# Optimization experiments

Measured on AMD Instinct MI355X. Metric: run time of the kernel, lower is better.

The kernel has to match this reference:

```python
import jax, jax.numpy as jnp
import numpy as np

T, D_IN, H, D_OUT = 20, 4, 768, 1
B = 1024


def setup_inputs() -> dict:
    key = jax.random.key(0)
    ks = jax.random.split(key, 8)
    s = 1.0 / np.sqrt(H)
    return {
        "batch_price": jax.random.normal(ks[0], (B, T, D_IN), jnp.float32),
        "batch_event": jax.random.normal(ks[1], (B, T, H), jnp.float32),
        "W_ih": jax.random.uniform(ks[2], (T, 4 * H, D_IN), jnp.float32, -s, s),
        "W_hh": jax.random.uniform(ks[3], (T, 4 * H, H), jnp.float32, -s, s),
        "b_ih": jax.random.uniform(ks[4], (T, 4 * H), jnp.float32, -s, s),
        "b_hh": jax.random.uniform(ks[5], (T, 4 * H), jnp.float32, -s, s),
        "fc_w": jax.random.uniform(ks[6], (D_OUT, H), jnp.float32, -s, s),
        "fc_b": jax.random.uniform(ks[7], (D_OUT,), jnp.float32, -s, s),
    }


def _lstm_cell(x, h_mat, c, wih, whh, bih, bhh):
    # gates: [B, 4H] in PyTorch LSTMCell order (i, f, g, o)
    gates = x @ wih.T + bih + h_mat @ whh.T + bhh
    i, f, g, o = jnp.split(gates, 4, axis=-1)
    c_next = jax.nn.sigmoid(f) * c + jax.nn.sigmoid(i) * jnp.tanh(g)
    h_next = jax.nn.sigmoid(o) * jnp.tanh(c_next)
    return h_next, c_next


def reference(batch_price, batch_event, W_ih, W_hh, b_ih, b_hh, fc_w, fc_b):
    Bb, Tt, _ = batch_price.shape
    Hh = W_hh.shape[-1]
    # step 0: hx = batch_event[:, 0], cell state = zeros
    h, c = _lstm_cell(batch_price[:, 0], batch_event[:, 0],
                      jnp.zeros((Bb, Hh), batch_price.dtype),
                      W_ih[0], W_hh[0], b_ih[0], b_hh[0])

    def step(carry, inp):
        h, c = carry
        x, ev, wih, whh, bih, bhh = inp
        # faithful to source: hx = torch.sum(batch_event_t + h_prev) -> scalar
        hx = jnp.sum(ev + h)
        h_mat = jnp.broadcast_to(hx, (Bb, Hh))
        h2, c2 = _lstm_cell(x, h_mat, c, wih, whh, bih, bhh)
        return (h2, c2), None

    xs = (jnp.swapaxes(batch_price[:, 1:], 0, 1),  # [T-1, B, D_IN]
          jnp.swapaxes(batch_event[:, 1:], 0, 1),  # [T-1, B, H]
          W_ih[1:], W_hh[1:], b_ih[1:], b_hh[1:])
    (h, c), _ = jax.lax.scan(step, (h, c), xs)
    return h @ fc_w.T + fc_b  # [B, 1]
```

## Files before the change

kernel.cpp:

```cpp
#include <hip/hip_runtime.h>
#include <stdint.h>

#define Bsz 1024
#define Tn  20
#define Hn  768
#define G4n 3072

#define WS_SH    0
#define WS_SEV   32
#define WS_PART  64
#define WS_BCAST 576
#define WS_RS    640
#define WS_BS    62080
#define WS_C     123520
#define WS_EVH   909952
#define WS_EVL   1303168
#define WS_WH    1696384
#define WS_WL    2581120

#define NBC_EV   512
#define NBC_W    1152
#define NBC_Z    3
#define NBC_TOT  (NBC_EV + NBC_W + NBC_Z)

#define NB_GEMM   768
#define NB_ROWSUM 1824
#define NB_SEV    608
#define NB_BIAS   60
#define NB_TOTAL  (NB_GEMM + NB_ROWSUM + NB_SEV + NB_BIAS)

typedef float  floatx4 __attribute__((ext_vector_type(4)));
typedef short  bfrag8  __attribute__((ext_vector_type(8)));

__device__ __forceinline__ float wave_reduce(float v){
#pragma unroll
    for (int o = 32; o > 0; o >>= 1) v += __shfl_down(v, o, 64);
    return v;
}
__device__ __forceinline__ float sigf(float x){ return 1.0f/(1.0f+__expf(-x)); }
__device__ __forceinline__ float tanhfast(float x){ return 2.0f/(1.0f+__expf(-2.0f*x)) - 1.0f; }
__device__ __forceinline__ unsigned short f2bf(float f){
    uint32_t u = __float_as_uint(f);
    return (unsigned short)((u + 0x7fffu + ((u>>16)&1u)) >> 16);
}
__device__ __forceinline__ float bf2f(unsigned short h){ return __uint_as_float(((uint32_t)h)<<16); }
__device__ __forceinline__ uint64_t pack_tv(unsigned t, float v){
    return ((uint64_t)t << 32) | (uint64_t)__float_as_uint(v);
}

__global__ __launch_bounds__(256) void k_conv(
    const float* __restrict__ ev, const float* __restrict__ whh,
    float* __restrict__ ws)
{
    int bid = blockIdx.x, tid = threadIdx.x;
    if (bid < NBC_EV + NBC_W) {
        if (tid >= 192) return;
        int r = tid / 96;
        int i = (tid - r*96) * 8;
        const float* src;
        unsigned short *dh, *dl;
        if (bid < NBC_EV) {
            int b = bid*2 + r;
            src = ev + (size_t)b*(Tn*Hn) + i;
            dh = (unsigned short*)(ws + WS_EVH) + (size_t)b*Hn + i;
            dl = (unsigned short*)(ws + WS_EVL) + (size_t)b*Hn + i;
        } else {
            int p = (bid - NBC_EV)*2 + r;
            int gsel = p / Hn;
            int ga = (gsel==0) ? 0 : (gsel==1 ? 2 : 3);
            int j = ga*Hn + (p - gsel*Hn);
            src = whh + (size_t)j*Hn + i;
            dh = (unsigned short*)(ws + WS_WH) + (size_t)p*Hn + i;
            dl = (unsigned short*)(ws + WS_WL) + (size_t)p*Hn + i;
        }
        float4 v0 = *(const float4*)src;
        float4 v1 = *(const float4*)(src+4);
        float f[8] = {v0.x,v0.y,v0.z,v0.w,v1.x,v1.y,v1.z,v1.w};
        bfrag8 hv, lv;
#pragma unroll
        for (int q = 0; q < 8; ++q) {
            unsigned short hb = f2bf(f[q]);
            hv[q] = (short)hb;
            lv[q] = (short)f2bf(f[q] - bf2f(hb));
        }
        *(bfrag8*)dh = hv;
        *(bfrag8*)dl = lv;
    } else {
        int idx = (bid - NBC_EV - NBC_W)*256 + tid;
        if (idx < 640) ws[idx] = 0.0f;
    }
}

__global__ __launch_bounds__(256) void k_pre(
    const float* __restrict__ price, const float* __restrict__ ev,
    const float* __restrict__ wih,   const float* __restrict__ whh,
    const float* __restrict__ bih,   const float* __restrict__ bhh,
    float* __restrict__ ws)
{
    __shared__ float redk[4];
    int blk = blockIdx.x, tid = threadIdx.x;
    int lane = tid & 63, wid = tid >> 6;

    if (blk < NB_GEMM) {
        float* Sh   = ws + WS_SH;
        float* cbuf = ws + WS_C;
        int bt = blk / 48, kt = blk % 48;
        int b0 = bt*64, k0 = kt*16;
        int w = wid, q = lane >> 4, col = lane & 15;

        const unsigned short* evh = (const unsigned short*)(ws + WS_EVH);
        const unsigned short* evl = (const unsigned short*)(ws + WS_EVL);
        const unsigned short* wh  = (const unsigned short*)(ws + WS_WH);
        const unsigned short* wl  = (const unsigned short*)(ws + WS_WL);

        int arow = b0 + w*16 + col;
        const unsigned short* pah = evh + (size_t)arow*Hn + q*8;
        const unsigned short* pal = evl + (size_t)arow*Hn + q*8;
        int br0 = 0*Hn + k0 + col;
        int br1 = 1*Hn + k0 + col;
        int br2 = 2*Hn + k0 + col;
        const unsigned short* pbh0 = wh + (size_t)br0*Hn + q*8;
        const unsigned short* pbl0 = wl + (size_t)br0*Hn + q*8;
        const unsigned short* pbh1 = wh + (size_t)br1*Hn + q*8;
        const unsigned short* pbl1 = wl + (size_t)br1*Hn + q*8;
        const unsigned short* pbh2 = wh + (size_t)br2*Hn + q*8;
        const unsigned short* pbl2 = wl + (size_t)br2*Hn + q*8;

        floatx4 acc0 = (floatx4){0.f,0.f,0.f,0.f};
        floatx4 acc1 = (floatx4){0.f,0.f,0.f,0.f};
        floatx4 acc2 = (floatx4){0.f,0.f,0.f,0.f};

#pragma unroll 4
        for (int kk = 0; kk < Hn; kk += 32) {
            bfrag8 ah = *(const bfrag8*)(pah + kk);
            bfrag8 al = *(const bfrag8*)(pal + kk);
            bfrag8 b0h = *(const bfrag8*)(pbh0 + kk);
            bfrag8 b0l = *(const bfrag8*)(pbl0 + kk);
            acc0 = __builtin_amdgcn_mfma_f32_16x16x32_bf16(ah, b0h, acc0, 0,0,0);
            acc0 = __builtin_amdgcn_mfma_f32_16x16x32_bf16(ah, b0l, acc0, 0,0,0);
            acc0 = __builtin_amdgcn_mfma_f32_16x16x32_bf16(al, b0h, acc0, 0,0,0);
            bfrag8 b1h = *(const bfrag8*)(pbh1 + kk);
            bfrag8 b1l = *(const bfrag8*)(pbl1 + kk);
            acc1 = __builtin_amdgcn_mfma_f32_16x16x32_bf16(ah, b1h, acc1, 0,0,0);
            acc1 = __builtin_amdgcn_mfma_f32_16x16x32_bf16(ah, b1l, acc1, 0,0,0);
            acc1 = __builtin_amdgcn_mfma_f32_16x16x32_bf16(al, b1h, acc1, 0,0,0);
            bfrag8 b2h = *(const bfrag8*)(pbh2 + kk);
            bfrag8 b2l = *(const bfrag8*)(pbl2 + kk);
            acc2 = __builtin_amdgcn_mfma_f32_16x16x32_bf16(ah, b2h, acc2, 0,0,0);
            acc2 = __builtin_amdgcn_mfma_f32_16x16x32_bf16(ah, b2l, acc2, 0,0,0);
            acc2 = __builtin_amdgcn_mfma_f32_16x16x32_bf16(al, b2h, acc2, 0,0,0);
        }

        float hsum = 0.f;
#pragma unroll
        for (int r = 0; r < 4; ++r) {
            int b = b0 + w*16 + q*4 + r;
            float4 xv = *(const float4*)(price + (size_t)b*(Tn*4));
            int j0 = 0*Hn + k0 + col;
            int j1 = 2*Hn + k0 + col;
            int j2 = 3*Hn + k0 + col;
            float4 w0 = *(const float4*)(wih + (size_t)j0*4);
            float4 w1 = *(const float4*)(wih + (size_t)j1*4);
            float4 w2 = *(const float4*)(wih + (size_t)j2*4);
            float gi = acc0[r] + xv.x*w0.x + xv.y*w0.y + xv.z*w0.z + xv.w*w0.w + bih[j0] + bhh[j0];
            float gg = acc1[r] + xv.x*w1.x + xv.y*w1.y + xv.z*w1.z + xv.w*w1.w + bih[j1] + bhh[j1];
            float go = acc2[r] + xv.x*w2.x + xv.y*w2.y + xv.z*w2.z + xv.w*w2.w + bih[j2] + bhh[j2];
            float c0 = sigf(gi) * tanhfast(gg);
            float h0 = sigf(go) * tanhfast(c0);
            cbuf[(size_t)b*Hn + k0 + col] = c0;
            hsum += h0;
        }
        hsum = wave_reduce(hsum);
        if (lane == 0) redk[w] = hsum;
        __syncthreads();
        if (tid == 0) atomicAdd(&Sh[0], redk[0]+redk[1]+redk[2]+redk[3]);
        return;
    }

    blk -= NB_GEMM;
    if (blk < NB_ROWSUM) {
        int gw = blk*4 + wid;
        int t  = 1 + gw/384;
        int j0 = (gw - (t-1)*384)*8;
        const float* base = whh + ((size_t)t*G4n + j0)*Hn + (size_t)lane*4;
        float s[8];
#pragma unroll
        for (int r = 0; r < 8; ++r) {
            float4 v0 = *(const float4*)(base + (size_t)r*Hn);
            float4 v1 = *(const float4*)(base + (size_t)r*Hn + 256);
            float4 v2 = *(const float4*)(base + (size_t)r*Hn + 512);
            s[r] = (v0.x+v0.y+v0.z+v0.w) + (v1.x+v1.y+v1.z+v1.w) + (v2.x+v2.y+v2.z+v2.w);
        }
        float* rowsum = ws + WS_RS;
#pragma unroll
        for (int r = 0; r < 8; ++r) {
            float rs = wave_reduce(s[r]);
            if (lane == 0) rowsum[(size_t)t*G4n + j0 + r] = rs;
        }
        return;
    }

    blk -= NB_ROWSUM;
    if (blk < NB_SEV) {
        int gw = blk*4 + wid;
        int t   = 1 + gw/128;
        int b0s = (gw - (t-1)*128)*8;
        float s = 0.f;
#pragma unroll
        for (int r = 0; r < 8; ++r) {
            const float* base = ev + ((size_t)(b0s+r)*Tn + t)*Hn + (size_t)lane*4;
            float4 v0 = *(const float4*)(base);
            float4 v1 = *(const float4*)(base + 256);
            float4 v2 = *(const float4*)(base + 512);
            s += (v0.x+v0.y+v0.z+v0.w) + (v1.x+v1.y+v1.z+v1.w) + (v2.x+v2.y+v2.z+v2.w);
        }
        s = wave_reduce(s);
        if (lane == 0) atomicAdd(ws + WS_SEV + t, s);
        return;
    }

    blk -= NB_SEV;
    {
        int idx = blk*256 + tid;
        float4 a = *(const float4*)(bih + (size_t)idx*4);
        float4 b = *(const float4*)(bhh + (size_t)idx*4);
        float4 r4; r4.x=a.x+b.x; r4.y=a.y+b.y; r4.z=a.z+b.z; r4.w=a.w+b.w;
        *(float4*)(ws + WS_BS + (size_t)idx*4) = r4;
    }
}

__global__ __launch_bounds__(768) void k_steps(
    const float* __restrict__ price, const float* __restrict__ wih,
    const float* __restrict__ fcw,   const float* __restrict__ fcb,
    float* __restrict__ ws, float* __restrict__ out)
{
    __shared__ float pr[4][80];
    __shared__ float red[12];
    __shared__ float redP[4];
    __shared__ float redF[4][12];

    float* Sh  = ws + WS_SH;
    float* Sev = ws + WS_SEV;
    uint64_t* part = (uint64_t*)(ws + WS_PART);
    const float* rowsum  = ws + WS_RS;
    const float* biassum = ws + WS_BS;
    float* cbuf = ws + WS_C;

    int blk = blockIdx.x, tid = threadIdx.x;
    int lane = tid & 63, wid = tid >> 6;
    int k = tid;

    if (tid < 320) {
        int e = tid / 80, r = tid - e*80;
        pr[e][r] = price[(size_t)(blk + 256*e)*(Tn*4) + r];
    }

    float c[4];
#pragma unroll
    for (int e = 0; e < 4; ++e)
        c[e] = cbuf[(size_t)(blk + 256*e)*Hn + k];

    float fcwk = fcw[k];
    float fcb0 = fcb[0];
    float sh0  = Sh[0];

    __syncthreads();

    float hsum_prev = 0.f;
    float vout[4] = {0.f,0.f,0.f,0.f};

    for (int t = 1; t < Tn; ++t) {
        if (t >= 2) {
            float v = wave_reduce(hsum_prev);
            if (lane == 0) red[wid] = v;
            __syncthreads();
            if (tid == 0) {
                float tot = 0.f;
#pragma unroll
                for (int i = 0; i < 12; ++i) tot += red[i];
                __hip_atomic_store(&part[blk], pack_tv((unsigned)(t-1), tot),
                                   __ATOMIC_RELAXED, __HIP_MEMORY_SCOPE_AGENT);
            }
        }

        const float* wih_t = wih + (size_t)t*G4n*4;
        float rsv[4], base[4][4];
#pragma unroll
        for (int g = 0; g < 4; ++g) {
            int j = g*Hn + k;
            float4 wv = *(const float4*)(wih_t + (size_t)j*4);
            rsv[g]   = rowsum[t*G4n + j];
            float bs = biassum[t*G4n + j];
#pragma unroll
            for (int e = 0; e < 4; ++e) {
                base[e][g] = pr[e][t*4+0]*wv.x + pr[e][t*4+1]*wv.y
                           + pr[e][t*4+2]*wv.z + pr[e][t*4+3]*wv.w + bs;
            }
        }
        float sevt = Sev[t];

        float hx;
        if (t == 1) {
            hx = sevt + sh0;
        } else {
            if (tid < 256) {
                uint64_t u = __hip_atomic_load(&part[tid], __ATOMIC_RELAXED, __HIP_MEMORY_SCOPE_AGENT);
                while ((unsigned)(u >> 32) != (unsigned)(t-1)) {
                    __builtin_amdgcn_s_sleep(1);
                    u = __hip_atomic_load(&part[tid], __ATOMIC_RELAXED, __HIP_MEMORY_SCOPE_AGENT);
                }
                float pv = wave_reduce(__uint_as_float((uint32_t)u));
                if (lane == 0) redP[wid] = pv;
            }
            __syncthreads();
            hx = sevt + (redP[0]+redP[1]+redP[2]+redP[3]);
        }

        float hsum = 0.f;
#pragma unroll
        for (int e = 0; e < 4; ++e) {
            float gi = base[e][0] + hx*rsv[0];
            float gf = base[e][1] + hx*rsv[1];
            float gg = base[e][2] + hx*rsv[2];
            float go = base[e][3] + hx*rsv[3];
            float cn = sigf(gf)*c[e] + sigf(gi)*tanhfast(gg);
            c[e] = cn;
            float h = sigf(go)*tanhfast(cn);
            hsum += h;
            if (t == Tn-1) vout[e] = wave_reduce(h * fcwk);
        }
        hsum_prev = hsum;
    }

    if (lane == 0) {
#pragma unroll
        for (int e = 0; e < 4; ++e) redF[e][wid] = vout[e];
    }
    __syncthreads();
    if (tid < 4) {
        float tot = 0.f;
#pragma unroll
        for (int i = 0; i < 12; ++i) tot += redF[tid][i];
        out[blk + 256*tid] = tot + fcb0;
    }
}

extern "C" void kernel_launch(void* const* d_in, const int* in_sizes, int n_in,
                              void* d_out, int out_size, void* d_ws, size_t ws_size,
                              hipStream_t stream)
{
    const float* price = (const float*)d_in[0];
    const float* ev    = (const float*)d_in[1];
    const float* wih   = (const float*)d_in[2];
    const float* whh   = (const float*)d_in[3];
    const float* bih   = (const float*)d_in[4];
    const float* bhh   = (const float*)d_in[5];
    const float* fcw   = (const float*)d_in[6];
    const float* fcb   = (const float*)d_in[7];
    float* out = (float*)d_out;
    float* ws  = (float*)d_ws;

    k_conv <<<NBC_TOT, 256, 0, stream>>>(ev, whh, ws);
    k_pre  <<<NB_TOTAL, 256, 0, stream>>>(price, ev, wih, whh, bih, bhh, ws);
    k_steps<<<256, 768, 0, stream>>>(price, wih, fcw, fcb, ws, out);
}
```

Measured before the change: 475.2 us.

## Broadcast per-step hx from one block and tile GEMM operands for MFMA

Before, every block of the step kernel polled all 256 partial-sum slots and reduced them itself. Now only block 0 gathers the partials and publishes the packed (step, hx) value through a single broadcast slot, and the other blocks spin on that one word, without sleeps. The bf16 split copies of the event and weight matrices are also stored in an MFMA-fragment-tiled layout, so each wave reads its operand fragments contiguously, and the W_ih and bias loads are hoisted out of the per-row epilogue loop. The broadcast adds a serial hop through block 0 on every step, and tight polling without sleep adds pressure on the memory system.

```diff
diff --git a/kernel.cpp b/kernel.cpp
--- a/kernel.cpp
+++ b/kernel.cpp
@@ -59,32 +59,38 @@
         int i = (tid - r*96) * 8;
         const float* src;
         unsigned short *dh, *dl;
+        int prow;
         if (bid < NBC_EV) {
-            int b = bid*2 + r;
-            src = ev + (size_t)b*(Tn*Hn) + i;
-            dh = (unsigned short*)(ws + WS_EVH) + (size_t)b*Hn + i;
-            dl = (unsigned short*)(ws + WS_EVL) + (size_t)b*Hn + i;
+            prow = bid*2 + r;
+            src = ev + (size_t)prow*(Tn*Hn) + i;
+            dh = (unsigned short*)(ws + WS_EVH);
+            dl = (unsigned short*)(ws + WS_EVL);
         } else {
             int p = (bid - NBC_EV)*2 + r;
             int gsel = p / Hn;
             int ga = (gsel==0) ? 0 : (gsel==1 ? 2 : 3);
             int j = ga*Hn + (p - gsel*Hn);
+            prow = p;
             src = whh + (size_t)j*Hn + i;
-            dh = (unsigned short*)(ws + WS_WH) + (size_t)p*Hn + i;
-            dl = (unsigned short*)(ws + WS_WL) + (size_t)p*Hn + i;
-        }
+            dh = (unsigned short*)(ws + WS_WH);
+            dl = (unsigned short*)(ws + WS_WL);
+        }
+        int rb = prow >> 4, col = prow & 15;
+        int kb = i >> 5, q = (i >> 3) & 3;
+        size_t base = (((size_t)(rb*24 + kb))*64 + q*16 + col) * 8;
+
         float4 v0 = *(const float4*)src;
         float4 v1 = *(const float4*)(src+4);
         float f[8] = {v0.x,v0.y,v0.z,v0.w,v1.x,v1.y,v1.z,v1.w};
         bfrag8 hv, lv;
 #pragma unroll
-        for (int q = 0; q < 8; ++q) {
-            unsigned short hb = f2bf(f[q]);
-            hv[q] = (short)hb;
-            lv[q] = (short)f2bf(f[q] - bf2f(hb));
-        }
-        *(bfrag8*)dh = hv;
-        *(bfrag8*)dl = lv;
+        for (int qq = 0; qq < 8; ++qq) {
+            unsigned short hb = f2bf(f[qq]);
+            hv[qq] = (short)hb;
+            lv[qq] = (short)f2bf(f[qq] - bf2f(hb));
+        }
+        *(bfrag8*)(dh + base) = hv;
+        *(bfrag8*)(dl + base) = lv;
     } else {
         int idx = (bid - NBC_EV - NBC_W)*256 + tid;
         if (idx < 640) ws[idx] = 0.0f;
@@ -113,58 +119,60 @@
         const unsigned short* wh  = (const unsigned short*)(ws + WS_WH);
         const unsigned short* wl  = (const unsigned short*)(ws + WS_WL);
 
-        int arow = b0 + w*16 + col;
-        const unsigned short* pah = evh + (size_t)arow*Hn + q*8;
-        const unsigned short* pal = evl + (size_t)arow*Hn + q*8;
-        int br0 = 0*Hn + k0 + col;
-        int br1 = 1*Hn + k0 + col;
-        int br2 = 2*Hn + k0 + col;
-        const unsigned short* pbh0 = wh + (size_t)br0*Hn + q*8;
-        const unsigned short* pbl0 = wl + (size_t)br0*Hn + q*8;
-        const unsigned short* pbh1 = wh + (size_t)br1*Hn + q*8;
-        const unsigned short* pbl1 = wl + (size_t)br1*Hn + q*8;
-        const unsigned short* pbh2 = wh + (size_t)br2*Hn + q*8;
-        const unsigned short* pbl2 = wl + (size_t)br2*Hn + q*8;
+        int rb_a = bt*4 + w;
+        const unsigned short* pah = evh + (size_t)rb_a*24*512 + (size_t)lane*8;
+        const unsigned short* pal = evl + (size_t)rb_a*24*512 + (size_t)lane*8;
+        const unsigned short* pb0h = wh + (size_t)(  0 + kt)*24*512 + (size_t)lane*8;
+        const unsigned short* pb0l = wl + (size_t)(  0 + kt)*24*512 + (size_t)lane*8;
+        const unsigned short* pb1h = wh + (size_t)( 48 + kt)*24*512 + (size_t)lane*8;
+        const unsigned short* pb1l = wl + (size_t)( 48 + kt)*24*512 + (size_t)lane*8;
+        const unsigned short* pb2h = wh + (size_t)( 96 + kt)*24*512 + (size_t)lane*8;
+        const unsigned short* pb2l = wl + (size_t)( 96 + kt)*24*512 + (size_t)lane*8;
 
         floatx4 acc0 = (floatx4){0.f,0.f,0.f,0.f};
         floatx4 acc1 = (floatx4){0.f,0.f,0.f,0.f};
         floatx4 acc2 = (floatx4){0.f,0.f,0.f,0.f};
 
 #pragma unroll 4
-        for (int kk = 0; kk < Hn; kk += 32) {
-            bfrag8 ah = *(const bfrag8*)(pah + kk);
-            bfrag8 al = *(const bfrag8*)(pal + kk);
-            bfrag8 b0h = *(const bfrag8*)(pbh0 + kk);
-            bfrag8 b0l = *(const bfrag8*)(pbl0 + kk);
+        for (int kb = 0; kb < 24; ++kb) {
+            int off = kb*512;
+            bfrag8 ah  = *(const bfrag8*)(pah  + off);
+            bfrag8 al  = *(const bfrag8*)(pal  + off);
+            bfrag8 b0h = *(const bfrag8*)(pb0h + off);
+            bfrag8 b0l = *(const bfrag8*)(pb0l + off);
             acc0 = __builtin_amdgcn_mfma_f32_16x16x32_bf16(ah, b0h, acc0, 0,0,0);
             acc0 = __builtin_amdgcn_mfma_f32_16x16x32_bf16(ah, b0l, acc0, 0,0,0);
             acc0 = __builtin_amdgcn_mfma_f32_16x16x32_bf16(al, b0h, acc0, 0,0,0);
-            bfrag8 b1h = *(const bfrag8*)(pbh1 + kk);
-            bfrag8 b1l = *(const bfrag8*)(pbl1 + kk);
+            bfrag8 b1h = *(const bfrag8*)(pb1h + off);
+            bfrag8 b1l = *(const bfrag8*)(pb1l + off);
             acc1 = __builtin_amdgcn_mfma_f32_16x16x32_bf16(ah, b1h, acc1, 0,0,0);
             acc1 = __builtin_amdgcn_mfma_f32_16x16x32_bf16(ah, b1l, acc1, 0,0,0);
             acc1 = __builtin_amdgcn_mfma_f32_16x16x32_bf16(al, b1h, acc1, 0,0,0);
-            bfrag8 b2h = *(const bfrag8*)(pbh2 + kk);
-            bfrag8 b2l = *(const bfrag8*)(pbl2 + kk);
+            bfrag8 b2h = *(const bfrag8*)(pb2h + off);
+            bfrag8 b2l = *(const bfrag8*)(pb2l + off);
             acc2 = __builtin_amdgcn_mfma_f32_16x16x32_bf16(ah, b2h, acc2, 0,0,0);
             acc2 = __builtin_amdgcn_mfma_f32_16x16x32_bf16(ah, b2l, acc2, 0,0,0);
             acc2 = __builtin_amdgcn_mfma_f32_16x16x32_bf16(al, b2h, acc2, 0,0,0);
         }
 
+        int j0 = 0*Hn + k0 + col;
+        int j1 = 2*Hn + k0 + col;
+        int j2 = 3*Hn + k0 + col;
+        float4 w0 = *(const float4*)(wih + (size_t)j0*4);
+        float4 w1 = *(const float4*)(wih + (size_t)j1*4);
+        float4 w2 = *(const float4*)(wih + (size_t)j2*4);
+        float bb0 = bih[j0] + bhh[j0];
+        float bb1 = bih[j1] + bhh[j1];
+        float bb2 = bih[j2] + bhh[j2];
+
         float hsum = 0.f;
 #pragma unroll
         for (int r = 0; r < 4; ++r) {
             int b = b0 + w*16 + q*4 + r;
             float4 xv = *(const float4*)(price + (size_t)b*(Tn*4));
-            int j0 = 0*Hn + k0 + col;
-            int j1 = 2*Hn + k0 + col;
-            int j2 = 3*Hn + k0 + col;
-            float4 w0 = *(const float4*)(wih + (size_t)j0*4);
-            float4 w1 = *(const float4*)(wih + (size_t)j1*4);
-            float4 w2 = *(const float4*)(wih + (size_t)j2*4);
-            float gi = acc0[r] + xv.x*w0.x + xv.y*w0.y + xv.z*w0.z + xv.w*w0.w + bih[j0] + bhh[j0];
-            float gg = acc1[r] + xv.x*w1.x + xv.y*w1.y + xv.z*w1.z + xv.w*w1.w + bih[j1] + bhh[j1];
-            float go = acc2[r] + xv.x*w2.x + xv.y*w2.y + xv.z*w2.z + xv.w*w2.w + bih[j2] + bhh[j2];
+            float gi = acc0[r] + xv.x*w0.x + xv.y*w0.y + xv.z*w0.z + xv.w*w0.w + bb0;
+            float gg = acc1[r] + xv.x*w1.x + xv.y*w1.y + xv.z*w1.z + xv.w*w1.w + bb1;
+            float go = acc2[r] + xv.x*w2.x + xv.y*w2.y + xv.z*w2.z + xv.w*w2.w + bb2;
             float c0 = sigf(gi) * tanhfast(gg);
             float h0 = sigf(go) * tanhfast(c0);
             cbuf[(size_t)b*Hn + k0 + col] = c0;
@@ -238,10 +246,12 @@
     __shared__ float red[12];
     __shared__ float redP[4];
     __shared__ float redF[4][12];
+    __shared__ float shx;
 
     float* Sh  = ws + WS_SH;
     float* Sev = ws + WS_SEV;
-    uint64_t* part = (uint64_t*)(ws + WS_PART);
+    uint64_t* part  = (uint64_t*)(ws + WS_PART);
+    uint64_t* bcast = (uint64_t*)(ws + WS_BCAST);
     const float* rowsum  = ws + WS_RS;
     const float* biassum = ws + WS_BS;
     float* cbuf = ws + WS_C;
@@ -299,22 +309,41 @@
         }
         float sevt = Sev[t];
 
-        float hx;
-        if (t == 1) {
-            hx = sevt + sh0;
-        } else {
-            if (tid < 256) {
-                uint64_t u = __hip_atomic_load(&part[tid], __ATOMIC_RELAXED, __HIP_MEMORY_SCOPE_AGENT);
-                while ((unsigned)(u >> 32) != (unsigned)(t-1)) {
-                    __builtin_amdgcn_s_sleep(1);
-                    u = __hip_atomic_load(&part[tid], __ATOMIC_RELAXED, __HIP_MEMORY_SCOPE_AGENT);
+        if (blk == 0) {
+            if (t >= 2) {
+                if (tid < 256) {
+                    uint64_t u;
+                    do { u = __hip_atomic_load(&part[tid], __ATOMIC_RELAXED, __HIP_MEMORY_SCOPE_AGENT); }
+                    while ((unsigned)(u >> 32) != (unsigned)(t-1));
+                    float pv = wave_reduce(__uint_as_float((uint32_t)u));
+                    if (lane == 0) redP[wid] = pv;
                 }
-                float pv = wave_reduce(__uint_as_float((uint32_t)u));
-                if (lane == 0) redP[wid] = pv;
+                __syncthreads();
+                if (tid == 0) {
+                    float hx = sevt + (redP[0]+redP[1]+redP[2]+redP[3]);
+                    shx = hx;
+                    __hip_atomic_store(bcast, pack_tv((unsigned)t, hx),
+                                       __ATOMIC_RELAXED, __HIP_MEMORY_SCOPE_AGENT);
+                }
+            } else {
+                if (tid == 0) {
+                    float hx = sevt + sh0;
+                    shx = hx;
+                    __hip_atomic_store(bcast, pack_tv(1u, hx),
+                                       __ATOMIC_RELAXED, __HIP_MEMORY_SCOPE_AGENT);
+                }
             }
             __syncthreads();
-            hx = sevt + (redP[0]+redP[1]+redP[2]+redP[3]);
-        }
+        } else {
+            if (tid == 0) {
+                uint64_t u;
+                do { u = __hip_atomic_load(bcast, __ATOMIC_RELAXED, __HIP_MEMORY_SCOPE_AGENT); }
+                while ((unsigned)(u >> 32) != (unsigned)t);
+                shx = __uint_as_float((uint32_t)u);
+            }
+            __syncthreads();
+        }
+        float hx = shx;
 
         float hsum = 0.f;
 #pragma unroll
```

After: 428.1 us. 1.11x faster.
